# Kernel tuning notes

Measured on AMD Instinct MI355X. Metric: run time of the kernel, lower is better.

## Reference

```python
import jax, jax.numpy as jnp
import numpy as np

T, D, H = 65536, 256, 256


def setup_inputs() -> dict:
    key = jax.random.key(0)
    ks = jax.random.split(key, 6)
    lim = 1.0 / np.sqrt(H)  # equinox GRUCell init: U(-1/sqrt(hidden), 1/sqrt(hidden))
    x = jax.random.normal(ks[0], (T, D), dtype=jnp.float32)
    state = jnp.zeros((H,), dtype=jnp.float32)
    start = jax.random.randint(ks[1], (T,), 0, 2).astype(jnp.int32)  # episode-start mask
    next_done = jnp.zeros((T,), dtype=jnp.int32)  # unused by forward, kept for signature fidelity
    W_ih = jax.random.uniform(ks[2], (3 * H, D), minval=-lim, maxval=lim, dtype=jnp.float32)
    W_hh = jax.random.uniform(ks[3], (3 * H, H), minval=-lim, maxval=lim, dtype=jnp.float32)
    bias = jax.random.uniform(ks[4], (3 * H,), minval=-lim, maxval=lim, dtype=jnp.float32)
    bias_n = jax.random.uniform(ks[5], (H,), minval=-lim, maxval=lim, dtype=jnp.float32)
    return {"x": x, "state": state, "start": start, "next_done": next_done,
            "W_ih": W_ih, "W_hh": W_hh, "bias": bias, "bias_n": bias_n}


def reference(x, state, start, next_done, W_ih, W_hh, bias, bias_n):
    # Input-dependent gate pre-activations for all timesteps in one big GEMM: [T, 3H]
    igates_all = x @ W_ih.T + bias
    start_f = start.astype(x.dtype)

    def step(h, inp):
        ig, s = inp
        h = h * (1.0 - s)  # reset hidden at episode start (state * logical_not(start))
        hg = W_hh @ h  # [3H]
        r = jax.nn.sigmoid(ig[:H] + hg[:H])
        z = jax.nn.sigmoid(ig[H:2 * H] + hg[H:2 * H])
        n = jnp.tanh(ig[2 * H:] + r * (hg[2 * H:] + bias_n))
        new_h = n + z * (h - n)  # equinox GRUCell output
        return new_h, new_h

    final_state, y = jax.lax.scan(step, state, (igates_all, start_f))
    return y, final_state
```

## Files before the change

### kernel.cpp

```cpp
#include <hip/hip_runtime.h>
#include <hip/hip_bf16.h>
#include <stdint.h>

#define TT   65536
#define NCH  16
#define CNOM 16
#define NBLK 256
#define ROWB 1664

typedef __bf16 bf16x8 __attribute__((ext_vector_type(8)));
typedef float  f32x4  __attribute__((ext_vector_type(4)));
typedef int    i32x4  __attribute__((ext_vector_type(4)));

__device__ __bf16 g_whh[768 * 256];
__device__ __align__(64) unsigned char g_ig[(size_t)TT * ROWB];

__device__ __forceinline__ float bfbits(uint32_t u) {
  float f; __builtin_memcpy(&f, &u, 4); return f;
}

__device__ __forceinline__ void mfma_bv0(f32x4& acc, bf16x8 a, i32x4 b) {
  asm("v_mfma_f32_16x16x32_bf16 %0, %1, %2, 0" : "=&v"(acc) : "v"(a), "v"(b));
}
__device__ __forceinline__ void mfma_ba0(f32x4& acc, bf16x8 a, i32x4 b) {
  asm("v_mfma_f32_16x16x32_bf16 %0, %1, %2, 0" : "=&v"(acc) : "v"(a), "a"(b));
}
__device__ __forceinline__ void mfma_bv(f32x4& acc, bf16x8 a, i32x4 b) {
  asm("v_mfma_f32_16x16x32_bf16 %0, %1, %2, %0" : "+v"(acc) : "v"(a), "v"(b));
}
__device__ __forceinline__ void mfma_ba(f32x4& acc, bf16x8 a, i32x4 b) {
  asm("v_mfma_f32_16x16x32_bf16 %0, %1, %2, %0" : "+v"(acc) : "v"(a), "a"(b));
}

__device__ __forceinline__ bf16x8 cvt8(float4 f0, float4 f1) {
  bf16x8 v;
  v[0] = (__bf16)f0.x; v[1] = (__bf16)f0.y; v[2] = (__bf16)f0.z; v[3] = (__bf16)f0.w;
  v[4] = (__bf16)f1.x; v[5] = (__bf16)f1.y; v[6] = (__bf16)f1.z; v[7] = (__bf16)f1.w;
  return v;
}

__global__ void prep_w(const float* __restrict__ whh) {
  const int n = 768 * 256;
  for (int i = blockIdx.x * blockDim.x + threadIdx.x; i < n; i += gridDim.x * blockDim.x)
    g_whh[i] = (__bf16)whh[i];
}

__global__ __launch_bounds__(512) void gemm_ig(const float* __restrict__ x,
                                               const float* __restrict__ wih,
                                               const float* __restrict__ bias) {
  __shared__ __align__(16) __bf16 a_s[4][128 * 64];
  __shared__ __align__(16) __bf16 b_s[2][128 * 64];
  const int tid = threadIdx.x;
  const int lane = tid & 63, l15 = lane & 15, q = lane >> 4;
  const int w = tid >> 6;
  const int wm = w >> 2, wn = w & 3;
  const int m0 = blockIdx.x * 128;

  float bvA[6], bvB[6];
#pragma unroll
  for (int nb = 0; nb < 6; ++nb) {
    bvA[nb] = bias[nb * 128 + wn * 32 + l15];
    bvB[nb] = bias[nb * 128 + wn * 32 + 16 + l15];
  }

#pragma unroll
  for (int kc = 0; kc < 4; ++kc)
#pragma unroll
    for (int i = 0; i < 2; ++i) {
      int pslot = i * 512 + tid;
      int row = pslot >> 3, c = pslot & 7, cs = c ^ (row & 7);
      const float* xs = x + (size_t)(m0 + row) * 256 + kc * 64 + cs * 8;
      float4 f0 = *(const float4*)xs;
      float4 f1 = *(const float4*)(xs + 4);
      *(bf16x8*)((char*)a_s[kc] + pslot * 16) = cvt8(f0, f1);
    }
#pragma unroll
  for (int i = 0; i < 2; ++i) {
    int pslot = i * 512 + tid;
    int row = pslot >> 3, c = pslot & 7, cs = c ^ (row & 7);
    const float* ws = wih + (size_t)(row) * 256 + cs * 8;
    float4 f0 = *(const float4*)ws;
    float4 f1 = *(const float4*)(ws + 4);
    *(bf16x8*)((char*)b_s[0] + pslot * 16) = cvt8(f0, f1);
  }

  f32x4 acc[4][2];
#pragma unroll
  for (int a = 0; a < 4; ++a)
#pragma unroll
    for (int b = 0; b < 2; ++b) acc[a][b] = (f32x4){0.f, 0.f, 0.f, 0.f};
  __syncthreads();

#pragma unroll
  for (int ntb = 0; ntb < 6; ++ntb) {
#pragma unroll
    for (int kc = 0; kc < 4; ++kc) {
      const int ci = ntb * 4 + kc;
      const int buf = ci & 1;
      const int nn = (ci + 1) >> 2, kk = (ci + 1) & 3;
      const bool more = (ci + 1) < 24;
      float4 wf00, wf01, wf10, wf11;
      if (more) {
        int ps0 = tid, r0 = ps0 >> 3, cs0 = (ps0 & 7) ^ (r0 & 7);
        const float* ws0 = wih + (size_t)(nn * 128 + r0) * 256 + kk * 64 + cs0 * 8;
        wf00 = *(const float4*)ws0; wf01 = *(const float4*)(ws0 + 4);
        int ps1 = 512 + tid, r1 = ps1 >> 3, cs1 = (ps1 & 7) ^ (r1 & 7);
        const float* ws1 = wih + (size_t)(nn * 128 + r1) * 256 + kk * 64 + cs1 * 8;
        wf10 = *(const float4*)ws1; wf11 = *(const float4*)(ws1 + 4);
      }
#pragma unroll
      for (int ks = 0; ks < 2; ++ks) {
        bf16x8 af[4], bfr[2];
#pragma unroll
        for (int tm = 0; tm < 4; ++tm) {
          int row = wm * 64 + tm * 16 + l15;
          int cb = (ks * 4 + q) ^ (row & 7);
          af[tm] = *(const bf16x8*)((const char*)a_s[kc] + row * 128 + cb * 16);
        }
#pragma unroll
        for (int tn = 0; tn < 2; ++tn) {
          int row = wn * 32 + tn * 16 + l15;
          int cb = (ks * 4 + q) ^ (row & 7);
          bfr[tn] = *(const bf16x8*)((const char*)b_s[buf] + row * 128 + cb * 16);
        }
#pragma unroll
        for (int tm = 0; tm < 4; ++tm)
#pragma unroll
          for (int tn = 0; tn < 2; ++tn)
            acc[tm][tn] = __builtin_amdgcn_mfma_f32_16x16x32_bf16(af[tm], bfr[tn], acc[tm][tn], 0, 0, 0);
      }
      if (more) {
        *(bf16x8*)((char*)b_s[buf ^ 1] + tid * 16) = cvt8(wf00, wf01);
        *(bf16x8*)((char*)b_s[buf ^ 1] + (512 + tid) * 16) = cvt8(wf10, wf11);
      }
      if (kc == 3) {
#pragma unroll
        for (int tm = 0; tm < 4; ++tm)
#pragma unroll
          for (int r = 0; r < 4; ++r) {
            int t = m0 + wm * 64 + tm * 16 + q * 4 + r;
            __bf16 lo = (__bf16)(acc[tm][0][r] + bvA[ntb]);
            __bf16 hi = (__bf16)(acc[tm][1][r] + bvB[ntb]);
            unsigned short ulo, uhi;
            __builtin_memcpy(&ulo, &lo, 2); __builtin_memcpy(&uhi, &hi, 2);
            uint32_t u = (uint32_t)ulo | ((uint32_t)uhi << 16);
            *(uint32_t*)(g_ig + (size_t)t * ROWB + ntb * 256 + wn * 64 + l15 * 4) = u;
          }
#pragma unroll
        for (int a = 0; a < 4; ++a)
#pragma unroll
          for (int b = 0; b < 2; ++b) acc[a][b] = (f32x4){0.f, 0.f, 0.f, 0.f};
      }
      __syncthreads();
    }
  }
}

__global__ __launch_bounds__(512)
__attribute__((amdgpu_waves_per_eu(2, 2)))
void gru_scan(const float* __restrict__ state, const int* __restrict__ start,
              const float* __restrict__ bias_n, float* __restrict__ out) {
  __shared__ __align__(16) __bf16 h_s[2][16][264];
  __shared__ __align__(16) unsigned char whh_lds[8 * 16 * 1024];
  __shared__ int flg_s[16 * 132];
  __shared__ int s_arr[17];

  const int tid = threadIdx.x;
  const int w = tid >> 6, lane = tid & 63, l15 = lane & 15, q = lane >> 4;
  const int jrow0 = w * 32 + l15;

  if (tid < 17) {
    int t = (blockIdx.x * NCH + tid) * CNOM;
    if (t > 0) { while (t < TT && start[t] == 0) t++; }
    s_arr[tid] = t;
  }
  for (int i = tid; i < 16 * 264; i += 512) (&h_s[0][0][0])[i] = (__bf16)0.f;
  __syncthreads();

  int sa[4], len[4];
#pragma unroll
  for (int r = 0; r < 4; ++r) {
    sa[r] = s_arr[q * 4 + r];
    len[r] = s_arr[q * 4 + r + 1] - sa[r];
  }
  int ML = 0;
  for (int m = 0; m < 16; ++m) { int L = s_arr[m + 1] - s_arr[m]; ML = L > ML ? L : ML; }
  ML = __builtin_amdgcn_readfirstlane(ML);

  for (int idx = tid; idx < 2048; idx += 512) {
    int m = idx >> 7, kk = idx & 127;
    int t = s_arr[m] + kk;
    flg_s[m * 132 + kk] = (t < TT) ? start[t] : 0;
  }

  char* lp = (char*)whh_lds + w * 16384 + lane * 16;
#pragma unroll
  for (int p = 0; p < 2; ++p)
#pragma unroll
    for (int ks = 0; ks < 8; ++ks) {
      i32x4 t = *(const i32x4*)&g_whh[(size_t)(w * 32 + p * 16 + l15) * 256 + q * 8 + ks * 32];
      *(i32x4*)(lp + (p * 8 + ks) * 1024) = t;
    }
  i32x4 whh_z[2][8], whh_n[2][8];
#pragma unroll
  for (int p = 0; p < 2; ++p)
#pragma unroll
    for (int ks = 0; ks < 8; ++ks) {
      whh_z[p][ks] = *(const i32x4*)&g_whh[(size_t)(1 * 256 + w * 32 + p * 16 + l15) * 256 + q * 8 + ks * 32];
      whh_n[p][ks] = *(const i32x4*)&g_whh[(size_t)(2 * 256 + w * 32 + p * 16 + l15) * 256 + q * 8 + ks * 32];
    }
#pragma unroll
  for (int p = 0; p < 2; ++p)
#pragma unroll
    for (int ks = 0; ks < 8; ++ks) {
      asm volatile("" : "+a"(whh_z[p][ks]));
      asm volatile("" : "+a"(whh_n[p][ks]));
    }

  const float bn2[2] = { bias_n[jrow0], bias_n[jrow0 + 16] };

  const int start0 = start[0];
  if (blockIdx.x == 0 && tid < 256) h_s[0][0][tid] = start0 ? (__bf16)0.f : (__bf16)state[tid];

  float hreg[2][4];
#pragma unroll
  for (int p = 0; p < 2; ++p)
#pragma unroll
    for (int r = 0; r < 4; ++r) hreg[p][r] = 0.f;
  if (blockIdx.x == 0 && q == 0 && !start0) {
    hreg[0][0] = state[jrow0];
    hreg[1][0] = state[jrow0 + 16];
  }

  const int cw = (w >> 2) * 256 + ((w & 3) * 16 + l15) * 4;
  const uint32_t offlim = (uint32_t)(TT - 1) * ROWB + (uint32_t)cw;
  uint32_t off[4];
  float* op[4];
#pragma unroll
  for (int r = 0; r < 4; ++r) {
    off[r] = (uint32_t)sa[r] * ROWB + (uint32_t)cw;
    op[r] = out + (size_t)sa[r] * 256 + jrow0;
  }

  const unsigned char* gig = g_ig;
  uint32_t igA[12], igB[12];
#pragma unroll
  for (int r = 0; r < 4; ++r) {
    igA[r * 3 + 0] = *(const uint32_t*)(gig + off[r]);
    igA[r * 3 + 1] = *(const uint32_t*)(gig + off[r] + 512);
    igA[r * 3 + 2] = *(const uint32_t*)(gig + off[r] + 1024);
    uint32_t nx = off[r] + ROWB; off[r] = nx > offlim ? offlim : nx;
  }
  __syncthreads();

  auto step = [&](int k, uint32_t (&cur)[12], uint32_t (&nxt)[12]) {
#pragma unroll
    for (int r = 0; r < 4; ++r) {
      nxt[r * 3 + 0] = *(const uint32_t*)(gig + off[r]);
      nxt[r * 3 + 1] = *(const uint32_t*)(gig + off[r] + 512);
      nxt[r * 3 + 2] = *(const uint32_t*)(gig + off[r] + 1024);
      uint32_t nx = off[r] + ROWB; off[r] = nx > offlim ? offlim : nx;
    }
    int fnext[4];
    if (k + 1 < 128) {
#pragma unroll
      for (int r = 0; r < 4; ++r) fnext[r] = flg_s[(q * 4 + r) * 132 + k + 1];
    } else {
#pragma unroll
      for (int r = 0; r < 4; ++r) {
        int t = sa[r] + k + 1; t = t > TT - 1 ? TT - 1 : t;
        fnext[r] = start[t];
      }
    }

    const __bf16* hb = &h_s[k & 1][0][0] + l15 * 264 + q * 8;
#pragma unroll
    for (int p = 0; p < 2; ++p) {
      f32x4 a0, a1, a2;
      {
        bf16x8 hf = *(const bf16x8*)(hb);
        i32x4 b0 = *(const i32x4*)(lp + (p * 8) * 1024);
        mfma_bv0(a0, hf, b0);
        mfma_ba0(a1, hf, whh_z[p][0]);
        mfma_ba0(a2, hf, whh_n[p][0]);
      }
#pragma unroll
      for (int ks = 1; ks < 8; ++ks) {
        bf16x8 hf = *(const bf16x8*)(hb + ks * 32);
        i32x4 b0 = *(const i32x4*)(lp + (p * 8 + ks) * 1024);
        mfma_bv(a0, hf, b0);
        mfma_ba(a1, hf, whh_z[p][ks]);
        mfma_ba(a2, hf, whh_n[p][ks]);
      }
      asm volatile("s_nop 7\n\ts_nop 7" : "+v"(a0), "+v"(a1), "+v"(a2));
#pragma unroll
      for (int r = 0; r < 4; ++r) {
        uint32_t vr = cur[r * 3 + 0];
        uint32_t vz = cur[r * 3 + 1];
        uint32_t vn = cur[r * 3 + 2];
        float igr = bfbits(p ? (vr & 0xffff0000u) : (vr << 16));
        float igz = bfbits(p ? (vz & 0xffff0000u) : (vz << 16));
        float ign = bfbits(p ? (vn & 0xffff0000u) : (vn << 16));
        float rp_ = a0[r] + igr;
        float zp_ = a1[r] + igz;
        float hv  = a2[r] + bn2[p];
        float rg = 1.f / (1.f + __expf(-rp_));
        float zg = 1.f / (1.f + __expf(-zp_));
        float np = ign + rg * hv;
        np = fminf(fmaxf(np, -30.f), 30.f);
        float e2 = __expf(2.f * np);
        float ng = (e2 - 1.f) / (e2 + 1.f);
        float hn = ng + zg * (hreg[p][r] - ng);
        if (k < len[r]) op[r][p * 16] = hn;
        hreg[p][r] = fnext[r] ? 0.f : hn;
      }
    }
    __bf16* hw = &h_s[(k + 1) & 1][0][0];
#pragma unroll
    for (int p = 0; p < 2; ++p)
#pragma unroll
      for (int r = 0; r < 4; ++r)
        hw[(q * 4 + r) * 264 + jrow0 + p * 16] = (__bf16)hreg[p][r];
#pragma unroll
    for (int r = 0; r < 4; ++r) op[r] += 256;
    asm volatile("s_waitcnt lgkmcnt(0)" ::: "memory");
    __builtin_amdgcn_s_barrier();
  };

  for (int k = 0; k < ML; ) {
    step(k, igA, igB); ++k;
    if (k < ML) { step(k, igB, igA); ++k; }
  }
}

__global__ void fin_copy(float* __restrict__ out) {
  int i = threadIdx.x;
  out[(size_t)TT * 256 + i] = out[((size_t)TT - 1) * 256 + i];
}

extern "C" void kernel_launch(void* const* d_in, const int* in_sizes, int n_in,
                              void* d_out, int out_size, void* d_ws, size_t ws_size,
                              hipStream_t stream) {
  const float* x      = (const float*)d_in[0];
  const float* state  = (const float*)d_in[1];
  const int*   start  = (const int*)d_in[2];
  const float* wih    = (const float*)d_in[4];
  const float* whh    = (const float*)d_in[5];
  const float* bias   = (const float*)d_in[6];
  const float* bias_n = (const float*)d_in[7];
  float* out = (float*)d_out;

  prep_w<<<256, 256, 0, stream>>>(whh);
  gemm_ig<<<512, 512, 0, stream>>>(x, wih, bias);
  gru_scan<<<NBLK, 512, 0, stream>>>(state, start, bias_n, out);
  fin_copy<<<1, 256, 0, stream>>>(out);
}
```

Before: 281.8 us.

## Fold weight prep and final-state copy into GEMM and scan kernels

Removes the separate prep_w and fin_copy launches. The W_hh bf16 conversion moves into the GEMM kernel, and the scan writes the final state directly when it reaches the last timestep. The GEMM is retiled to 64-row blocks with 256 threads and 1024 blocks, and it uses nontemporal loads for x and nontemporal stores for the outputs. This cuts launch overhead and changes GEMM occupancy, at the cost of fewer rows per block and therefore more W_ih reloads.

```diff
diff --git a/kernel.cpp b/kernel.cpp
--- a/kernel.cpp
+++ b/kernel.cpp
@@ -32,56 +32,53 @@
   asm("v_mfma_f32_16x16x32_bf16 %0, %1, %2, %0" : "+v"(acc) : "v"(a), "a"(b));
 }
 
-__device__ __forceinline__ bf16x8 cvt8(float4 f0, float4 f1) {
+__device__ __forceinline__ bf16x8 cvt8v(f32x4 f0, f32x4 f1) {
   bf16x8 v;
-  v[0] = (__bf16)f0.x; v[1] = (__bf16)f0.y; v[2] = (__bf16)f0.z; v[3] = (__bf16)f0.w;
-  v[4] = (__bf16)f1.x; v[5] = (__bf16)f1.y; v[6] = (__bf16)f1.z; v[7] = (__bf16)f1.w;
+  v[0] = (__bf16)f0[0]; v[1] = (__bf16)f0[1]; v[2] = (__bf16)f0[2]; v[3] = (__bf16)f0[3];
+  v[4] = (__bf16)f1[0]; v[5] = (__bf16)f1[1]; v[6] = (__bf16)f1[2]; v[7] = (__bf16)f1[3];
   return v;
 }
 
-__global__ void prep_w(const float* __restrict__ whh) {
-  const int n = 768 * 256;
-  for (int i = blockIdx.x * blockDim.x + threadIdx.x; i < n; i += gridDim.x * blockDim.x)
-    g_whh[i] = (__bf16)whh[i];
-}
-
-__global__ __launch_bounds__(512) void gemm_ig(const float* __restrict__ x,
+__global__ __launch_bounds__(256) void gemm_ig(const float* __restrict__ x,
                                                const float* __restrict__ wih,
+                                               const float* __restrict__ whh,
                                                const float* __restrict__ bias) {
-  __shared__ __align__(16) __bf16 a_s[4][128 * 64];
+  __shared__ __align__(16) __bf16 a_s[4][64 * 64];
   __shared__ __align__(16) __bf16 b_s[2][128 * 64];
   const int tid = threadIdx.x;
   const int lane = tid & 63, l15 = lane & 15, q = lane >> 4;
   const int w = tid >> 6;
-  const int wm = w >> 2, wn = w & 3;
-  const int m0 = blockIdx.x * 128;
+  const int m0 = blockIdx.x * 64;
+
+  {
+    int i = blockIdx.x * 256 + tid;
+    if (i < 768 * 256) g_whh[i] = (__bf16)whh[i];
+  }
 
   float bvA[6], bvB[6];
 #pragma unroll
   for (int nb = 0; nb < 6; ++nb) {
-    bvA[nb] = bias[nb * 128 + wn * 32 + l15];
-    bvB[nb] = bias[nb * 128 + wn * 32 + 16 + l15];
+    bvA[nb] = bias[nb * 128 + w * 32 + l15];
+    bvB[nb] = bias[nb * 128 + w * 32 + 16 + l15];
   }
 
 #pragma unroll
   for (int kc = 0; kc < 4; ++kc)
 #pragma unroll
     for (int i = 0; i < 2; ++i) {
-      int pslot = i * 512 + tid;
+      int pslot = i * 256 + tid;
       int row = pslot >> 3, c = pslot & 7, cs = c ^ (row & 7);
-      const float* xs = x + (size_t)(m0 + row) * 256 + kc * 64 + cs * 8;
-      float4 f0 = *(const float4*)xs;
-      float4 f1 = *(const float4*)(xs + 4);
-      *(bf16x8*)((char*)a_s[kc] + pslot * 16) = cvt8(f0, f1);
-    }
-#pragma unroll
-  for (int i = 0; i < 2; ++i) {
-    int pslot = i * 512 + tid;
+      const f32x4* xs = (const f32x4*)(x + (size_t)(m0 + row) * 256 + kc * 64 + cs * 8);
+      f32x4 f0 = __builtin_nontemporal_load(xs);
+      f32x4 f1 = __builtin_nontemporal_load(xs + 1);
+      *(bf16x8*)((char*)a_s[kc] + pslot * 16) = cvt8v(f0, f1);
+    }
+#pragma unroll
+  for (int it = 0; it < 4; ++it) {
+    int pslot = it * 256 + tid;
     int row = pslot >> 3, c = pslot & 7, cs = c ^ (row & 7);
-    const float* ws = wih + (size_t)(row) * 256 + cs * 8;
-    float4 f0 = *(const float4*)ws;
-    float4 f1 = *(const float4*)(ws + 4);
-    *(bf16x8*)((char*)b_s[0] + pslot * 16) = cvt8(f0, f1);
+    const f32x4* ws = (const f32x4*)(wih + (size_t)row * 256 + cs * 8);
+    *(bf16x8*)((char*)b_s[0] + pslot * 16) = cvt8v(ws[0], ws[1]);
   }
 
   f32x4 acc[4][2];
@@ -91,68 +88,65 @@
     for (int b = 0; b < 2; ++b) acc[a][b] = (f32x4){0.f, 0.f, 0.f, 0.f};
   __syncthreads();
 
-#pragma unroll
-  for (int ntb = 0; ntb < 6; ++ntb) {
-#pragma unroll
-    for (int kc = 0; kc < 4; ++kc) {
-      const int ci = ntb * 4 + kc;
-      const int buf = ci & 1;
-      const int nn = (ci + 1) >> 2, kk = (ci + 1) & 3;
-      const bool more = (ci + 1) < 24;
-      float4 wf00, wf01, wf10, wf11;
-      if (more) {
-        int ps0 = tid, r0 = ps0 >> 3, cs0 = (ps0 & 7) ^ (r0 & 7);
-        const float* ws0 = wih + (size_t)(nn * 128 + r0) * 256 + kk * 64 + cs0 * 8;
-        wf00 = *(const float4*)ws0; wf01 = *(const float4*)(ws0 + 4);
-        int ps1 = 512 + tid, r1 = ps1 >> 3, cs1 = (ps1 & 7) ^ (r1 & 7);
-        const float* ws1 = wih + (size_t)(nn * 128 + r1) * 256 + kk * 64 + cs1 * 8;
-        wf10 = *(const float4*)ws1; wf11 = *(const float4*)(ws1 + 4);
-      }
-#pragma unroll
-      for (int ks = 0; ks < 2; ++ks) {
-        bf16x8 af[4], bfr[2];
-#pragma unroll
-        for (int tm = 0; tm < 4; ++tm) {
-          int row = wm * 64 + tm * 16 + l15;
-          int cb = (ks * 4 + q) ^ (row & 7);
-          af[tm] = *(const bf16x8*)((const char*)a_s[kc] + row * 128 + cb * 16);
+  for (int ci = 0; ci < 24; ++ci) {
+    const int ntb = ci >> 2, kc = ci & 3, buf = ci & 1;
+    const int nn = (ci + 1) >> 2, kk = (ci + 1) & 3;
+    const bool more = (ci + 1) < 24;
+    f32x4 wf0[4], wf1[4];
+    if (more) {
+#pragma unroll
+      for (int it = 0; it < 4; ++it) {
+        int pslot = it * 256 + tid;
+        int row = pslot >> 3, c = pslot & 7, cs = c ^ (row & 7);
+        const f32x4* ws = (const f32x4*)(wih + (size_t)(nn * 128 + row) * 256 + kk * 64 + cs * 8);
+        wf0[it] = ws[0]; wf1[it] = ws[1];
+      }
+    }
+#pragma unroll
+    for (int ks = 0; ks < 2; ++ks) {
+      bf16x8 af[4], bfr[2];
+#pragma unroll
+      for (int tm = 0; tm < 4; ++tm) {
+        int row = tm * 16 + l15;
+        int cb = (ks * 4 + q) ^ (row & 7);
+        af[tm] = *(const bf16x8*)((const char*)a_s[kc] + row * 128 + cb * 16);
+      }
+#pragma unroll
+      for (int tn = 0; tn < 2; ++tn) {
+        int row = w * 32 + tn * 16 + l15;
+        int cb = (ks * 4 + q) ^ (row & 7);
+        bfr[tn] = *(const bf16x8*)((const char*)b_s[buf] + row * 128 + cb * 16);
+      }
+#pragma unroll
+      for (int tm = 0; tm < 4; ++tm)
+#pragma unroll
+        for (int tn = 0; tn < 2; ++tn)
+          acc[tm][tn] = __builtin_amdgcn_mfma_f32_16x16x32_bf16(af[tm], bfr[tn], acc[tm][tn], 0, 0, 0);
+    }
+    if (more) {
+#pragma unroll
+      for (int it = 0; it < 4; ++it)
+        *(bf16x8*)((char*)b_s[buf ^ 1] + (it * 256 + tid) * 16) = cvt8v(wf0[it], wf1[it]);
+    }
+    if (kc == 3) {
+#pragma unroll
+      for (int tm = 0; tm < 4; ++tm)
+#pragma unroll
+        for (int r = 0; r < 4; ++r) {
+          int t = m0 + tm * 16 + q * 4 + r;
+          __bf16 lo = (__bf16)(acc[tm][0][r] + bvA[ntb]);
+          __bf16 hi = (__bf16)(acc[tm][1][r] + bvB[ntb]);
+          unsigned short ulo, uhi;
+          __builtin_memcpy(&ulo, &lo, 2); __builtin_memcpy(&uhi, &hi, 2);
+          uint32_t u = (uint32_t)ulo | ((uint32_t)uhi << 16);
+          *(uint32_t*)(g_ig + (size_t)t * ROWB + ntb * 256 + w * 64 + l15 * 4) = u;
         }
 #pragma unroll
-        for (int tn = 0; tn < 2; ++tn) {
-          int row = wn * 32 + tn * 16 + l15;
-          int cb = (ks * 4 + q) ^ (row & 7);
-          bfr[tn] = *(const bf16x8*)((const char*)b_s[buf] + row * 128 + cb * 16);
-        }
-#pragma unroll
-        for (int tm = 0; tm < 4; ++tm)
-#pragma unroll
-          for (int tn = 0; tn < 2; ++tn)
-            acc[tm][tn] = __builtin_amdgcn_mfma_f32_16x16x32_bf16(af[tm], bfr[tn], acc[tm][tn], 0, 0, 0);
-      }
-      if (more) {
-        *(bf16x8*)((char*)b_s[buf ^ 1] + tid * 16) = cvt8(wf00, wf01);
-        *(bf16x8*)((char*)b_s[buf ^ 1] + (512 + tid) * 16) = cvt8(wf10, wf11);
-      }
-      if (kc == 3) {
-#pragma unroll
-        for (int tm = 0; tm < 4; ++tm)
-#pragma unroll
-          for (int r = 0; r < 4; ++r) {
-            int t = m0 + wm * 64 + tm * 16 + q * 4 + r;
-            __bf16 lo = (__bf16)(acc[tm][0][r] + bvA[ntb]);
-            __bf16 hi = (__bf16)(acc[tm][1][r] + bvB[ntb]);
-            unsigned short ulo, uhi;
-            __builtin_memcpy(&ulo, &lo, 2); __builtin_memcpy(&uhi, &hi, 2);
-            uint32_t u = (uint32_t)ulo | ((uint32_t)uhi << 16);
-            *(uint32_t*)(g_ig + (size_t)t * ROWB + ntb * 256 + wn * 64 + l15 * 4) = u;
-          }
-#pragma unroll
-        for (int a = 0; a < 4; ++a)
-#pragma unroll
-          for (int b = 0; b < 2; ++b) acc[a][b] = (f32x4){0.f, 0.f, 0.f, 0.f};
-      }
-      __syncthreads();
-    }
+      for (int a = 0; a < 4; ++a)
+#pragma unroll
+        for (int b = 0; b < 2; ++b) acc[a][b] = (f32x4){0.f, 0.f, 0.f, 0.f};
+    }
+    __syncthreads();
   }
 }
 
@@ -311,7 +305,11 @@
         float e2 = __expf(2.f * np);
         float ng = (e2 - 1.f) / (e2 + 1.f);
         float hn = ng + zg * (hreg[p][r] - ng);
-        if (k < len[r]) op[r][p * 16] = hn;
+        if (k < len[r]) {
+          __builtin_nontemporal_store(hn, &op[r][p * 16]);
+          if (sa[r] + k == TT - 1)
+            __builtin_nontemporal_store(hn, out + (size_t)TT * 256 + jrow0 + p * 16);
+        }
         hreg[p][r] = fnext[r] ? 0.f : hn;
       }
     }
@@ -331,11 +329,6 @@
     step(k, igA, igB); ++k;
     if (k < ML) { step(k, igB, igA); ++k; }
   }
-}
-
-__global__ void fin_copy(float* __restrict__ out) {
-  int i = threadIdx.x;
-  out[(size_t)TT * 256 + i] = out[((size_t)TT - 1) * 256 + i];
 }
 
 extern "C" void kernel_launch(void* const* d_in, const int* in_sizes, int n_in,
@@ -350,8 +343,6 @@
   const float* bias_n = (const float*)d_in[7];
   float* out = (float*)d_out;
 
-  prep_w<<<256, 256, 0, stream>>>(whh);
-  gemm_ig<<<512, 512, 0, stream>>>(x, wih, bias);
+  gemm_ig<<<1024, 256, 0, stream>>>(x, wih, whh, bias);
   gru_scan<<<NBLK, 512, 0, stream>>>(state, start, bias_n, out);
-  fin_copy<<<1, 256, 0, stream>>>(out);
-}
+}
```

Result: no change. 284.3 us (+0.9%).
